# Kernel optimization log

Measured on AMD Instinct MI355X. Metric: run time of the kernel, lower is better.

The kernel has to match this reference:

```python
import jax, jax.numpy as jnp
import numpy as np

N_NODES = 100000
N_EDGES = 1600000
N_GRAPHS = 512
N_REL = 4
N_TYPES = 13
EMB = 128
HID = 128
BN_EPS = 1e-5
L2_EPS = 1e-12


def setup_inputs() -> dict:
    key = jax.random.key(0)
    ks = jax.random.split(key, 16)
    node_type = jax.random.randint(ks[0], (N_NODES,), 0, N_TYPES)
    x = jax.nn.one_hot(node_type, N_TYPES, dtype=jnp.float32)  # [N,13] one-hot
    edge_index = jax.random.randint(ks[1], (2, N_EDGES), 0, N_NODES)
    edge_type = jax.random.randint(ks[2], (N_EDGES,), 0, N_REL)
    batch = jnp.sort(jax.random.randint(ks[3], (N_NODES,), 0, N_GRAPHS))
    s = 0.05
    return {
        "x": x,
        "edge_index": edge_index,
        "edge_type": edge_type,
        "batch": batch,
        "emb": jax.random.normal(ks[4], (N_TYPES, EMB), jnp.float32) * s,
        "Wrel": jax.random.normal(ks[5], (2, N_REL, HID, HID), jnp.float32) * s,  # layer0 in=EMB==HID
        "Wroot": jax.random.normal(ks[6], (2, HID, HID), jnp.float32) * s,
        "conv_bias": jnp.zeros((2, HID), jnp.float32),
        "bn_gamma": jnp.ones((2, HID), jnp.float32),
        "bn_beta": jnp.zeros((2, HID), jnp.float32),
        "prelu_a": jnp.full((2,), 0.25, jnp.float32),
        "fc1_w": jax.random.normal(ks[7], (HID, 256), jnp.float32) * s,
        "fc1_b": jnp.zeros((256,), jnp.float32),
        "fc2_w": jax.random.normal(ks[8], (256, 128), jnp.float32) * s,
        "fc2_b": jnp.zeros((128,), jnp.float32),
        "out_w": jax.random.normal(ks[9], (128, 1), jnp.float32) * s,
        "out_b": jnp.zeros((1,), jnp.float32),
    }


def _rgcn_conv(h, Wrel, Wroot, bias, src, dst, edge_type):
    # PyG RGCNConv: out = h @ Wroot + bias + sum_r mean_{edges of rel r}(h_src @ W_r)
    n = h.shape[0]
    out = h @ Wroot + bias
    for r in range(N_REL):
        m = (edge_type == r).astype(h.dtype)  # [E]
        hr = h @ Wrel[r]                       # [N, dout]
        msg = hr[src] * m[:, None]             # gather + mask  [E, dout]
        num = jax.ops.segment_sum(msg, dst, num_segments=n)
        cnt = jax.ops.segment_sum(m, dst, num_segments=n)
        out = out + num / jnp.maximum(cnt, 1.0)[:, None]
    return out


def _batchnorm(h, gamma, beta):
    mu = jnp.mean(h, axis=0)
    var = jnp.mean((h - mu) ** 2, axis=0)  # biased var (training-mode BN)
    return (h - mu) * jax.lax.rsqrt(var + BN_EPS) * gamma + beta


def reference(x, edge_index, edge_type, batch, emb, Wrel, Wroot, conv_bias,
              bn_gamma, bn_beta, prelu_a, fc1_w, fc1_b, fc2_w, fc2_b, out_w, out_b):
    src, dst = edge_index[0], edge_index[1]
    idx = jnp.argmax(x, axis=1)         # torch.nonzero(one_hot)[1]
    h = emb[idx]                        # [N, EMB]
    for l in range(2):
        h = _rgcn_conv(h, Wrel[l], Wroot[l], conv_bias[l], src, dst, edge_type)
        h = _batchnorm(h, bn_gamma[l], bn_beta[l])
        h = jnp.where(h >= 0, h, prelu_a[l] * h)  # PReLU
        nrm = jnp.sqrt(jnp.sum(h * h, axis=1, keepdims=True))
        h = h / jnp.maximum(nrm, L2_EPS)          # F.normalize(p=2, dim=1)
    # global mean pool over graphs
    pooled = jax.ops.segment_sum(h, batch, num_segments=N_GRAPHS)
    cnt = jax.ops.segment_sum(jnp.ones((h.shape[0],), h.dtype), batch, num_segments=N_GRAPHS)
    g = pooled / jnp.maximum(cnt, 1.0)[:, None]   # [G, HID]
    g = jax.nn.relu(g @ fc1_w + fc1_b)
    g = jax.nn.relu(g @ fc2_w + fc2_b)
    return g @ out_w + out_b                      # [G, 1]
```

## Files before the change

kernel.cpp:

```cpp
#include <hip/hip_runtime.h>
#include <hip/hip_bf16.h>

#define NN 100000
#define NE 1600000
#define NG 512
#define CH3 65536
#define CHW 16384
#define NCH 2
#define BPC 128
#define ES 12500


typedef __attribute__((ext_vector_type(8))) short short8;
typedef __attribute__((ext_vector_type(4))) float float4v;


__device__ inline int lower_bound_dev(const int* __restrict__ a, int n, int v) {
    int lo = 0, hi = n;
    while (lo < hi) { int mid = (lo + hi) >> 1; if (a[mid] < v) lo = mid + 1; else hi = mid; }
    return lo;
}

__device__ inline unsigned short f2bf(float x) {
    unsigned u = __float_as_uint(x);
    unsigned r = (u + 0x7fffu + ((u >> 16) & 1u)) >> 16;
    return (unsigned short)r;
}

__device__ inline float bf2f(unsigned short h) {
    return __uint_as_float((unsigned)h << 16);
}


__global__ void node_type_kernel(const float* __restrict__ x, int* __restrict__ idx, int n) {
    int i = blockIdx.x * blockDim.x + threadIdx.x;
    if (i >= n) return;
    const float* row = x + (size_t)i * 13;
    int b = 0;
    #pragma unroll
    for (int t = 0; t < 13; ++t) if (row[t] > 0.5f) { b = t; }
    idx[i] = b;
}

__global__ void pack_src_type(const int* __restrict__ src, const int* __restrict__ ntype,
                              int* __restrict__ srcT) {
    int e = blockIdx.x * 256 + threadIdx.x;
    if (e >= NE) return;
    int s = src[e];
    srcT[e] = s | (ntype[s] << 17);
}


__global__ __launch_bounds__(256) void hist_kernel(const int* __restrict__ dst,
                                                   unsigned* __restrict__ partials) {
    __shared__ unsigned h[CHW];
    const int b = blockIdx.x, c = blockIdx.y;
    const int lo = c * CH3;
    for (int i = threadIdx.x; i < CHW; i += 256) h[i] = 0;
    __syncthreads();
    const int e0 = b * ES;
    const int e1 = (e0 + ES < NE) ? e0 + ES : NE;
    for (int e = e0 + threadIdx.x; e < e1; e += 256) {
        int k = dst[e] - lo;
        if (k >= 0 && k < CH3) atomicAdd(&h[k >> 2], 1u << ((k & 3) << 3));
    }
    __syncthreads();
    unsigned* out = partials + ((size_t)(c * BPC + b)) * CHW;
    for (int i = threadIdx.x; i < CHW; i += 256) out[i] = h[i];
}

__global__ void hist_reduce(unsigned* __restrict__ partials, int* __restrict__ counts) {
    const int c = blockIdx.y;
    const int i = blockIdx.x * 256 + threadIdx.x;
    size_t base = (size_t)c * BPC * CHW + i;
    unsigned r0 = 0, r1 = 0, r2 = 0, r3 = 0;
    #pragma unroll 4
    for (int b = 0; b < BPC; ++b) {
        unsigned t = partials[base + (size_t)b * CHW];
        partials[base + (size_t)b * CHW] = r0 | (r1 << 8) | (r2 << 16) | (r3 << 24);
        r0 += t & 0xffu; r1 += (t >> 8) & 0xffu; r2 += (t >> 16) & 0xffu; r3 += t >> 24;
    }
    int k0 = c * CH3 + 4 * i;
    if (k0 < NN)     counts[k0]     = (int)r0;
    if (k0 + 1 < NN) counts[k0 + 1] = (int)r1;
    if (k0 + 2 < NN) counts[k0 + 2] = (int)r2;
    if (k0 + 3 < NN) counts[k0 + 3] = (int)r3;
}

__global__ __launch_bounds__(256) void scan1(const int* __restrict__ counts, int* __restrict__ offs,
                                             int* __restrict__ bsums, int n) {
    __shared__ int wsum[4];
    const int base = blockIdx.x * 1024 + threadIdx.x * 4;
    int v[4]; int loc = 0;
    #pragma unroll
    for (int j = 0; j < 4; ++j) { int idx = base + j; v[j] = (idx < n) ? counts[idx] : 0; loc += v[j]; }
    const int lane = threadIdx.x & 63, wid = threadIdx.x >> 6;
    int sc = loc;
    #pragma unroll
    for (int o = 1; o < 64; o <<= 1) { int t = __shfl_up(sc, o, 64); if (lane >= o) sc += t; }
    if (lane == 63) wsum[wid] = sc;
    __syncthreads();
    int wbase = 0;
    for (int w = 0; w < wid; ++w) wbase += wsum[w];
    int run = wbase + sc - loc;
    #pragma unroll
    for (int j = 0; j < 4; ++j) { int idx = base + j; if (idx < n) offs[idx] = run; run += v[j]; }
    if (threadIdx.x == 255) bsums[blockIdx.x] = wbase + sc;
}

__global__ void scan2(int* __restrict__ bsums, int* __restrict__ offs, int nb, int n) {
    const int lane = threadIdx.x;
    int carry = 0;
    for (int base = 0; base < nb; base += 64) {
        int idx = base + lane;
        int v = (idx < nb) ? bsums[idx] : 0;
        int sc = v;
        #pragma unroll
        for (int o = 1; o < 64; o <<= 1) { int t = __shfl_up(sc, o, 64); if (lane >= o) sc += t; }
        if (idx < nb) bsums[idx] = carry + sc - v;
        int tot = __shfl(sc, 63, 64);
        carry += tot;
    }
    if (lane == 0) offs[n] = carry;
}

__global__ __launch_bounds__(256) void scan3(int* __restrict__ offs, const int* __restrict__ bsums, int n) {
    const int s = bsums[blockIdx.x];
    const int base = blockIdx.x * 1024 + threadIdx.x * 4;
    #pragma unroll
    for (int j = 0; j < 4; ++j) { int idx = base + j; if (idx < n) offs[idx] += s; }
}

__global__ __launch_bounds__(256) void place_kernel(const int* __restrict__ dst,
                                                    const int* __restrict__ et,
                                                    const int* __restrict__ srcT,
                                                    const int* __restrict__ offs,
                                                    const unsigned* __restrict__ partials,
                                                    int* __restrict__ sortedSrc) {
    __shared__ unsigned cur[CHW];
    const int b = blockIdx.x, c = blockIdx.y;
    const int lo = c * CH3;
    const unsigned* pb = partials + ((size_t)(c * BPC + b)) * CHW;
    for (int i = threadIdx.x; i < CHW; i += 256) cur[i] = pb[i];
    __syncthreads();
    const int e0 = b * ES;
    const int e1 = (e0 + ES < NE) ? e0 + ES : NE;
    for (int e = e0 + threadIdx.x; e < e1; e += 256) {
        int key = dst[e];
        int k = key - lo;
        if (k >= 0 && k < CH3) {
            int sh = (k & 3) << 3;
            unsigned old = atomicAdd(&cur[k >> 2], 1u << sh);
            int my = (int)((old >> sh) & 0xffu);
            int pos = offs[key] + my;
            sortedSrc[pos] = srcT[e] | (et[e] << 21);
        }
    }
}


__global__ __launch_bounds__(256) void hist_A0(const int* __restrict__ sortedSrc,
                                               const int* __restrict__ offs,
                                               const int* __restrict__ ntype,
                                               unsigned short* __restrict__ A0) {
    __shared__ unsigned cnt[256][13];
    const int tid = threadIdx.x;
    const int n = blockIdx.x * 256 + tid;
    if (n >= NN) return;
    #pragma unroll
    for (int t = 0; t < 13; ++t) cnt[tid][t] = 0;
    const int o0 = offs[n], o1 = offs[n + 1];
    unsigned relc = 0;
    for (int i = o0; i < o1; ++i) {
        int v = sortedSrc[i];
        int ty = (v >> 17) & 15, r = v >> 21;
        cnt[tid][ty] += 1u << (r << 3);
        relc += 1u << (r << 3);
    }
    float inv[4];
    #pragma unroll
    for (int r = 0; r < 4; ++r) {
        unsigned c = (relc >> (r << 3)) & 0xffu;
        inv[r] = 1.0f / (float)(c > 0 ? c : 1);
    }
    const int myty = ntype[n];
    const int tile = n >> 4, l16 = n & 15;
    unsigned short* base = A0 + (size_t)tile * 1536 + l16 * 8;
    #pragma unroll
    for (int ks = 0; ks < 3; ++ks) {
        #pragma unroll
        for (int quad = 0; quad < 4; ++quad) {
            unsigned short vals[8];
            #pragma unroll
            for (int j = 0; j < 8; ++j) {
                int p = ks * 32 + quad * 8 + j;
                float v;
                if (p < 32) v = (p == myty) ? 1.0f : 0.0f;
                else {
                    int r = (p - 32) >> 4, tt = (p - 32) & 15;
                    v = (tt < 13) ? (float)((cnt[tid][tt] >> (r << 3)) & 0xffu) * inv[r] : 0.0f;
                }
                vals[j] = f2bf(v);
            }
            *(uint4*)(base + ks * 512 + quad * 128) = *(uint4*)vals;
        }
    }
}


__global__ void build_B0(const float* __restrict__ emb, const float* __restrict__ Wroot,
                         const float* __restrict__ Wrel, unsigned short* __restrict__ B0f,
                         float* __restrict__ bnSums) {
    if (blockIdx.x < 8) bnSums[blockIdx.x * 256 + threadIdx.x] = 0.f;
    int i = blockIdx.x * 256 + threadIdx.x;
    if (i >= 12288) return;
    int j = i & 7;
    int lane = (i >> 3) & 63;
    int t = (i >> 9) & 7;
    int ks = i >> 12;
    int n = t * 16 + (lane & 15);
    int p = ks * 32 + (lane >> 4) * 8 + j;
    float val = 0.f;
    if (p < 32) {
        if (p < 13) {
            const float* er = emb + (size_t)p * 128;
            const float* wc = Wroot + n;
            float acc = 0.f;
            for (int k = 0; k < 128; ++k) acc += er[k] * wc[(size_t)k * 128];
            val = acc;
        }
    } else {
        int r = (p - 32) >> 4, tt = (p - 32) & 15;
        if (tt < 13) {
            const float* er = emb + (size_t)tt * 128;
            const float* wc = Wrel + ((size_t)r * 128) * 128 + n;
            float acc = 0.f;
            for (int k = 0; k < 128; ++k) acc += er[k] * wc[(size_t)k * 128];
            val = acc;
        }
    }
    B0f[i] = f2bf(val);
}


__global__ void build_Bf1(const float* __restrict__ Wroot, const float* __restrict__ Wrel,
                          unsigned short* __restrict__ Bf, float* __restrict__ bnSums) {
    if (blockIdx.x < 8) bnSums[blockIdx.x * 256 + threadIdx.x] = 0.f;
    int i = blockIdx.x * 256 + threadIdx.x;
    if (i >= 81920) return;
    int j = i & 7;
    int lane = (i >> 3) & 63;
    int t = (i >> 9) & 7;
    int ks = (i >> 12) & 3;
    int kc = i >> 14;
    int n = t * 16 + (lane & 15);
    int kcol = j * 16 + ks * 4 + (lane >> 4);
    float w;
    if (kc == 0) w = Wroot[16384 + (size_t)kcol * 128 + n];
    else {
        int r = kc - 1;
        w = Wrel[(((size_t)(4 + r) * 128) + kcol) * 128 + n];
    }
    Bf[i] = f2bf(w);
}


__global__ __launch_bounds__(256) void gemm0_mfma(const unsigned short* __restrict__ A0,
                                                  const unsigned short* __restrict__ B0f,
                                                  const float* __restrict__ bias,
                                                  unsigned short* __restrict__ Cb,
                                                  float* __restrict__ bnSums, int M) {
    __shared__ float sred[2][4][128];
    const int tid = threadIdx.x;
    const int wv = tid >> 6, lane = tid & 63;
    const int l16 = lane & 15, quad = lane >> 4;
    const int rowbase = blockIdx.x * 128 + wv * 32;
    const int tmax = (M >> 4) - 1;
    int tile0 = blockIdx.x * 8 + wv * 2; if (tile0 > tmax) tile0 = tmax;
    int tile1 = tile0 + 1;               if (tile1 > tmax) tile1 = tmax;

    float4v acc[2][8];
    #pragma unroll
    for (int t = 0; t < 8; ++t) {
        float bv = bias[t * 16 + l16];
        float4v av = {bv, bv, bv, bv};
        acc[0][t] = av; acc[1][t] = av;
    }

    const unsigned short* bl = B0f + lane * 8;
    const unsigned short* F0 = A0 + (size_t)tile0 * 1536 + quad * 128 + l16 * 8;
    const unsigned short* F1 = A0 + (size_t)tile1 * 1536 + quad * 128 + l16 * 8;
    #pragma unroll
    for (int ks = 0; ks < 3; ++ks) {
        short8 af0 = *(const short8*)(F0 + ks * 512);
        short8 af1 = *(const short8*)(F1 + ks * 512);
        const unsigned short* bp = bl + ((ks * 8) << 9);
        #pragma unroll
        for (int t = 0; t < 8; ++t) {
            short8 bf = *(const short8*)(bp + (t << 9));
            acc[0][t] = __builtin_amdgcn_mfma_f32_16x16x32_bf16(af0, bf, acc[0][t], 0, 0, 0);
            acc[1][t] = __builtin_amdgcn_mfma_f32_16x16x32_bf16(af1, bf, acc[1][t], 0, 0, 0);
        }
    }

    #pragma unroll
    for (int h = 0; h < 2; ++h) {
        #pragma unroll
        for (int rg = 0; rg < 4; ++rg) {
            int rr = rowbase + h * 16 + quad * 4 + rg;
            if (rr < M) {
                unsigned short v[8];
                #pragma unroll
                for (int t = 0; t < 8; ++t) v[t] = f2bf(acc[h][t][rg]);
                *(uint4*)(Cb + (size_t)rr * 128 + l16 * 8) = *(uint4*)v;
            }
        }
    }
    float s[8], q[8];
    #pragma unroll
    for (int t = 0; t < 8; ++t) {
        s[t] = 0.f; q[t] = 0.f;
        #pragma unroll
        for (int h = 0; h < 2; ++h) {
            #pragma unroll
            for (int rg = 0; rg < 4; ++rg) {
                int rr = rowbase + h * 16 + quad * 4 + rg;
                if (rr < M) { float v = acc[h][t][rg]; s[t] += v; q[t] += v * v; }
            }
        }
    }
    #pragma unroll
    for (int t = 0; t < 8; ++t) {
        s[t] += __shfl_down(s[t], 32, 64); q[t] += __shfl_down(q[t], 32, 64);
        s[t] += __shfl_down(s[t], 16, 64); q[t] += __shfl_down(q[t], 16, 64);
    }
    if (lane < 16) {
        #pragma unroll
        for (int t = 0; t < 8; ++t) {
            sred[0][wv][t * 16 + l16] = s[t];
            sred[1][wv][t * 16 + l16] = q[t];
        }
    }
    __syncthreads();
    if (tid < 128) {
        float S = sred[0][0][tid] + sred[0][1][tid] + sred[0][2][tid] + sred[0][3][tid];
        float Q = sred[1][0][tid] + sred[1][1][tid] + sred[1][2][tid] + sred[1][3][tid];
        float* bnS = bnSums + ((blockIdx.x & 7) << 8);
        unsafeAtomicAdd(bnS + tid, S);
        unsafeAtomicAdd(bnS + 128 + tid, Q);
    }
}


__global__ __launch_bounds__(256) void gather_gemm1(const unsigned short* __restrict__ hbf,
                                                    const int* __restrict__ sortedSrc,
                                                    const int* __restrict__ offs,
                                                    const unsigned short* __restrict__ Bf,
                                                    const float* __restrict__ bias,
                                                    unsigned short* __restrict__ Cb,
                                                    float* __restrict__ bnSums) {
    __shared__ unsigned short rootL[2048];
    __shared__ unsigned short aggL[8192];
    const int tid = threadIdx.x;
    const int tile = blockIdx.x;
    {
        const int l16g = tid >> 4;
        const int cidx = tid & 15;
        const int c8 = cidx << 3;
        const int n = tile * 16 + l16g;
        const int pu = cidx * 16 + (l16g ^ cidx);
        uint4 ru = *(const uint4*)(hbf + (size_t)n * 128 + c8);
        *(uint4*)(rootL + pu * 8) = ru;

        const unsigned short* hb = hbf + c8;
        const int o0 = offs[n], o1 = offs[n + 1];

        float a0[8], a1[8], a2[8], a3[8];
        #pragma unroll
        for (int j = 0; j < 8; ++j) { a0[j] = 0.f; a1[j] = 0.f; a2[j] = 0.f; a3[j] = 0.f; }
        float c0 = 0.f, c1 = 0.f, c2 = 0.f, c3 = 0.f;

        auto body = [&](int v, uint4 u) {
            int r = v >> 21;
            float f[8];
            f[0] = __uint_as_float(u.x << 16); f[1] = __uint_as_float(u.x & 0xffff0000u);
            f[2] = __uint_as_float(u.y << 16); f[3] = __uint_as_float(u.y & 0xffff0000u);
            f[4] = __uint_as_float(u.z << 16); f[5] = __uint_as_float(u.z & 0xffff0000u);
            f[6] = __uint_as_float(u.w << 16); f[7] = __uint_as_float(u.w & 0xffff0000u);
            float m0 = (r == 0) ? 1.f : 0.f, m1 = (r == 1) ? 1.f : 0.f;
            float m2 = (r == 2) ? 1.f : 0.f, m3 = (r == 3) ? 1.f : 0.f;
            c0 += m0; c1 += m1; c2 += m2; c3 += m3;
            #pragma unroll
            for (int j = 0; j < 8; ++j) {
                a0[j] = fmaf(m0, f[j], a0[j]);
                a1[j] = fmaf(m1, f[j], a1[j]);
                a2[j] = fmaf(m2, f[j], a2[j]);
                a3[j] = fmaf(m3, f[j], a3[j]);
            }
        };

        int i = o0;
        for (; i + 4 <= o1; i += 4) {
            int v0 = sortedSrc[i], v1 = sortedSrc[i + 1];
            int v2 = sortedSrc[i + 2], v3 = sortedSrc[i + 3];
            uint4 u0 = *(const uint4*)(hb + (size_t)(v0 & 0x1ffff) * 128);
            uint4 u1 = *(const uint4*)(hb + (size_t)(v1 & 0x1ffff) * 128);
            uint4 u2 = *(const uint4*)(hb + (size_t)(v2 & 0x1ffff) * 128);
            uint4 u3 = *(const uint4*)(hb + (size_t)(v3 & 0x1ffff) * 128);
            body(v0, u0); body(v1, u1); body(v2, u2); body(v3, u3);
        }
        if (i + 2 <= o1) {
            int v0 = sortedSrc[i], v1 = sortedSrc[i + 1];
            uint4 u0 = *(const uint4*)(hb + (size_t)(v0 & 0x1ffff) * 128);
            uint4 u1 = *(const uint4*)(hb + (size_t)(v1 & 0x1ffff) * 128);
            body(v0, u0); body(v1, u1);
            i += 2;
        }
        if (i < o1) {
            int v0 = sortedSrc[i];
            uint4 u0 = *(const uint4*)(hb + (size_t)(v0 & 0x1ffff) * 128);
            body(v0, u0);
        }

        const float i0 = 1.f / fmaxf(c0, 1.f), i1 = 1.f / fmaxf(c1, 1.f);
        const float i2 = 1.f / fmaxf(c2, 1.f), i3 = 1.f / fmaxf(c3, 1.f);
        unsigned short* bp = aggL + pu * 8;
        auto pack = [&](float* a, float inv, unsigned short* dp) {
            unsigned short v[8];
            #pragma unroll
            for (int j = 0; j < 8; ++j) v[j] = f2bf(a[j] * inv);
            *(uint4*)dp = *(uint4*)v;
        };
        pack(a0, i0, bp);
        pack(a1, i1, bp + 2048);
        pack(a2, i2, bp + 4096);
        pack(a3, i3, bp + 6144);
    }
    __syncthreads();

    const int wv = tid >> 6, lane = tid & 63;
    const int l16 = lane & 15, quad = lane >> 4;
    const int t0 = wv << 1;
    float4v acc0, acc1;
    {
        float b0v = bias[t0 * 16 + l16];
        float b1v = bias[(t0 + 1) * 16 + l16];
        float4v a0v = {b0v, b0v, b0v, b0v};
        float4v a1v = {b1v, b1v, b1v, b1v};
        acc0 = a0v; acc1 = a1v;
    }
    const unsigned short* bl = Bf + lane * 8;
    #pragma unroll
    for (int kc = 0; kc < 5; ++kc) {
        const unsigned short* Abase = (kc == 0) ? rootL : (aggL + (kc - 1) * 2048);
        #pragma unroll
        for (int ks = 0; ks < 4; ++ks) {
            const int C = ks * 4 + quad;
            const int p = C * 16 + (l16 ^ C);
            short8 af = *(const short8*)(Abase + p * 8);
            const unsigned short* bp = bl + (((kc * 4 + ks) * 8 + t0) << 9);
            short8 b0 = *(const short8*)(bp);
            short8 b1 = *(const short8*)(bp + 512);
            acc0 = __builtin_amdgcn_mfma_f32_16x16x32_bf16(af, b0, acc0, 0, 0, 0);
            acc1 = __builtin_amdgcn_mfma_f32_16x16x32_bf16(af, b1, acc1, 0, 0, 0);
        }
    }
    const int rowbase = tile * 16;
    #pragma unroll
    for (int rg = 0; rg < 4; ++rg) {
        int rr = rowbase + quad * 4 + rg;
        unsigned pk = (unsigned)f2bf(acc0[rg]) | ((unsigned)f2bf(acc1[rg]) << 16);
        *(unsigned*)(Cb + (size_t)rr * 128 + l16 * 8 + t0) = pk;
    }
    float s0 = 0.f, q0 = 0.f, s1 = 0.f, q1 = 0.f;
    #pragma unroll
    for (int rg = 0; rg < 4; ++rg) {
        float v0 = acc0[rg], v1 = acc1[rg];
        s0 += v0; q0 += v0 * v0; s1 += v1; q1 += v1 * v1;
    }
    s0 += __shfl_down(s0, 32, 64); q0 += __shfl_down(q0, 32, 64);
    s1 += __shfl_down(s1, 32, 64); q1 += __shfl_down(q1, 32, 64);
    s0 += __shfl_down(s0, 16, 64); q0 += __shfl_down(q0, 16, 64);
    s1 += __shfl_down(s1, 16, 64); q1 += __shfl_down(q1, 16, 64);
    if (lane < 16) {
        float* bnS = bnSums + ((tile & 7) << 8);
        unsafeAtomicAdd(bnS + t0 * 16 + l16, s0);
        unsafeAtomicAdd(bnS + 128 + t0 * 16 + l16, q0);
        unsafeAtomicAdd(bnS + (t0 + 1) * 16 + l16, s1);
        unsafeAtomicAdd(bnS + 128 + (t0 + 1) * 16 + l16, q1);
    }
}


__global__ void bn_finalize(const float* __restrict__ bnSums, float* __restrict__ fin,
                            float* __restrict__ g0zero, int n) {
    const int c = threadIdx.x;
    if (g0zero) g0zero[blockIdx.x * 128 + c] = 0.f;
    if (blockIdx.x != 0) return;
    float s = 0.f, q = 0.f;
    #pragma unroll
    for (int j = 0; j < 8; ++j) { s += bnSums[j * 256 + c]; q += bnSums[j * 256 + 128 + c]; }
    const float invn = 1.0f / (float)n;
    float mu = s * invn;
    float var = q * invn - mu * mu; if (var < 0.f) var = 0.f;
    fin[c] = mu;
    fin[128 + c] = rsqrtf(var + 1e-5f);
}


__global__ __launch_bounds__(256) void bn_apply_kernel(const unsigned short* __restrict__ Cb,
                                unsigned short* __restrict__ hbf,
                                const float* __restrict__ fin,
                                const float* __restrict__ gamma, const float* __restrict__ beta,
                                const float* __restrict__ prelu_a, int layer) {
    const int tid = threadIdx.x;
    const int row = blockIdx.x * 16 + (tid >> 4);
    const int li = tid & 15;
    const int p8 = li << 3;
    const float a = prelu_a[layer];
    uint4 u = *(const uint4*)(Cb + (size_t)row * 128 + p8);
    float v[8];
    v[0] = __uint_as_float(u.x << 16); v[1] = __uint_as_float(u.x & 0xffff0000u);
    v[2] = __uint_as_float(u.y << 16); v[3] = __uint_as_float(u.y & 0xffff0000u);
    v[4] = __uint_as_float(u.z << 16); v[5] = __uint_as_float(u.z & 0xffff0000u);
    v[6] = __uint_as_float(u.w << 16); v[7] = __uint_as_float(u.w & 0xffff0000u);
    float t[8]; float ss = 0.f;
    #pragma unroll
    for (int j = 0; j < 8; ++j) {
        int cc = j * 16 + li;
        float tv = (v[j] - fin[cc]) * fin[128 + cc] * gamma[cc] + beta[cc];
        tv = (tv >= 0.f) ? tv : a * tv;
        t[j] = tv; ss += tv * tv;
    }
    ss += __shfl_xor(ss, 1, 64);
    ss += __shfl_xor(ss, 2, 64);
    ss += __shfl_xor(ss, 4, 64);
    ss += __shfl_xor(ss, 8, 64);
    const float scale = 1.0f / fmaxf(sqrtf(ss), 1e-12f);
    unsigned short o[8];
    #pragma unroll
    for (int j = 0; j < 8; ++j) o[j] = f2bf(t[j] * scale);
    *(uint4*)(hbf + (size_t)row * 128 + p8) = *(uint4*)o;
}


__global__ __launch_bounds__(256) void bn_apply_pool(const unsigned short* __restrict__ Cb,
                                const float* __restrict__ fin,
                                const float* __restrict__ gamma, const float* __restrict__ beta,
                                const float* __restrict__ prelu_a,
                                const int* __restrict__ batch,
                                float* __restrict__ g0) {
    __shared__ float P[16][128];
    __shared__ int gids[16];
    const int tid = threadIdx.x;
    const int r16 = tid >> 4;
    const int li = tid & 15;
    const int row = blockIdx.x * 16 + r16;
    const int p8 = li << 3;
    if (li == 0) gids[r16] = batch[row];
    const float a = prelu_a[1];
    uint4 u = *(const uint4*)(Cb + (size_t)row * 128 + p8);
    float v[8];
    v[0] = __uint_as_float(u.x << 16); v[1] = __uint_as_float(u.x & 0xffff0000u);
    v[2] = __uint_as_float(u.y << 16); v[3] = __uint_as_float(u.y & 0xffff0000u);
    v[4] = __uint_as_float(u.z << 16); v[5] = __uint_as_float(u.z & 0xffff0000u);
    v[6] = __uint_as_float(u.w << 16); v[7] = __uint_as_float(u.w & 0xffff0000u);
    float t[8]; float ss = 0.f;
    #pragma unroll
    for (int j = 0; j < 8; ++j) {
        int cc = j * 16 + li;
        float tv = (v[j] - fin[cc]) * fin[128 + cc] * gamma[cc] + beta[cc];
        tv = (tv >= 0.f) ? tv : a * tv;
        t[j] = tv; ss += tv * tv;
    }
    ss += __shfl_xor(ss, 1, 64);
    ss += __shfl_xor(ss, 2, 64);
    ss += __shfl_xor(ss, 4, 64);
    ss += __shfl_xor(ss, 8, 64);
    const float scale = 1.0f / fmaxf(sqrtf(ss), 1e-12f);
    #pragma unroll
    for (int j = 0; j < 8; ++j) P[r16][p8 + j] = t[j] * scale;
    __syncthreads();
    if (tid < 128) {
        int cur = gids[0];
        float run = 0.f;
        #pragma unroll
        for (int rr = 0; rr < 16; ++rr) {
            int g = gids[rr];
            if (g != cur) {
                unsafeAtomicAdd(&g0[(size_t)cur * 128 + tid], run);
                run = 0.f; cur = g;
            }
            run += P[rr][tid];
        }
        unsafeAtomicAdd(&g0[(size_t)cur * 128 + tid], run);
    }
}


__global__ void fc1_kernel(const float* __restrict__ g, const float* __restrict__ w,
                           const float* __restrict__ b, const int* __restrict__ batch,
                           float* __restrict__ o) {
    const int row = blockIdx.x;
    const int j = threadIdx.x;
    const int lo = lower_bound_dev(batch, NN, row);
    const int hi = lower_bound_dev(batch, NN, row + 1);
    const int c = hi - lo;
    const float invc = 1.0f / (float)(c > 0 ? c : 1);
    float acc = 0.f;
    #pragma unroll 8
    for (int k = 0; k < 128; ++k) {
        int lk = (k & 7) * 16 + (k >> 3);
        acc += g[row * 128 + k] * w[lk * 256 + j];
    }
    o[row * 256 + j] = fmaxf(acc * invc + b[j], 0.f);
}

__global__ void fc2_kernel(const float* __restrict__ g, const float* __restrict__ w,
                           const float* __restrict__ b, float* __restrict__ o) {
    const int row = blockIdx.x;
    const int j = threadIdx.x;
    float acc = b[j];
    #pragma unroll 8
    for (int k = 0; k < 256; ++k) acc += g[row * 256 + k] * w[k * 128 + j];
    o[row * 128 + j] = fmaxf(acc, 0.f);
}

__global__ void fco_kernel(const float* __restrict__ g, const float* __restrict__ w,
                           const float* __restrict__ b, float* __restrict__ o) {
    const int row = blockIdx.x * blockDim.x + threadIdx.x;
    if (row >= NG) return;
    float acc = b[0];
    #pragma unroll 8
    for (int k = 0; k < 128; ++k) acc += g[row * 128 + k] * w[k];
    o[row] = acc;
}


extern "C" void kernel_launch(void* const* d_in, const int* in_sizes, int n_in,
                              void* d_out, int out_size, void* d_ws, size_t ws_size,
                              hipStream_t stream) {
    const float* x      = (const float*)d_in[0];
    const int*   eidx   = (const int*)d_in[1];
    const int*   etype  = (const int*)d_in[2];
    const int*   batch  = (const int*)d_in[3];
    const float* emb    = (const float*)d_in[4];
    const float* Wrel   = (const float*)d_in[5];
    const float* Wroot  = (const float*)d_in[6];
    const float* cbias  = (const float*)d_in[7];
    const float* gamma  = (const float*)d_in[8];
    const float* beta   = (const float*)d_in[9];
    const float* prelua = (const float*)d_in[10];
    const float* fc1w   = (const float*)d_in[11];
    const float* fc1b   = (const float*)d_in[12];
    const float* fc2w   = (const float*)d_in[13];
    const float* fc2b   = (const float*)d_in[14];
    const float* outw   = (const float*)d_in[15];
    const float* outb   = (const float*)d_in[16];
    float* out = (float*)d_out;

    const int* src = eidx;
    const int* dst = eidx + NE;

    char* p = (char*)d_ws;
    auto alloc = [&](size_t bytes) { char* r = p; p += (bytes + 255) & ~(size_t)255; return r; };
    unsigned short* hbf   = (unsigned short*)alloc((size_t)NN * 128 * 2);
    unsigned short* Cb    = (unsigned short*)alloc((size_t)NN * 128 * 2);
    char*  scratch   = (char*)alloc((size_t)24 << 20);
    int*   sortedSrc = (int*)alloc((size_t)NE * 4);
    int*   srcT      = (int*)alloc((size_t)NE * 4);
    int*   offs      = (int*)alloc((size_t)(NN + 1) * 4);
    int*   bsums     = (int*)alloc(1024);
    int*   ntype     = (int*)alloc((size_t)NN * 4);
    unsigned short* Bf1 = (unsigned short*)alloc((size_t)81920 * 2);
    unsigned short* B0f = (unsigned short*)alloc((size_t)12288 * 2);
    float* bnSums  = (float*)alloc(2048 * 4);
    float* bnFin   = (float*)alloc(256 * 4);
    float* g0      = (float*)alloc((size_t)NG * 128 * 4);
    float* g1      = (float*)alloc((size_t)NG * 256 * 4);
    float* g2      = (float*)alloc((size_t)NG * 128 * 4);

    unsigned* partials = (unsigned*)scratch;
    unsigned short* A0 = (unsigned short*)scratch;

    const int NBLK = (NN + 1023) / 1024;

    node_type_kernel<<<(NN + 255) / 256, 256, 0, stream>>>(x, ntype, NN);
    pack_src_type<<<(NE + 255) / 256, 256, 0, stream>>>(src, ntype, srcT);

    hist_kernel<<<dim3(BPC, NCH), 256, 0, stream>>>(dst, partials);
    hist_reduce<<<dim3(CHW / 256, NCH), 256, 0, stream>>>(partials, offs);
    scan1<<<NBLK, 256, 0, stream>>>(offs, offs, bsums, NN);
    scan2<<<1, 64, 0, stream>>>(bsums, offs, NBLK, NN);
    scan3<<<NBLK, 256, 0, stream>>>(offs, bsums, NN);
    place_kernel<<<dim3(BPC, NCH), 256, 0, stream>>>(dst, etype, srcT, offs, partials, sortedSrc);

    hist_A0<<<(NN + 255) / 256, 256, 0, stream>>>(sortedSrc, offs, ntype, A0);

    build_B0<<<48, 256, 0, stream>>>(emb, Wroot, Wrel, B0f, bnSums);
    gemm0_mfma<<<(NN + 127) / 128, 256, 0, stream>>>(A0, B0f, cbias, Cb, bnSums, NN);
    bn_finalize<<<1, 128, 0, stream>>>(bnSums, bnFin, (float*)nullptr, NN);
    bn_apply_kernel<<<NN / 16, 256, 0, stream>>>(Cb, hbf, bnFin, gamma, beta, prelua, 0);

    build_Bf1<<<320, 256, 0, stream>>>(Wroot, Wrel, Bf1, bnSums);
    gather_gemm1<<<NN / 16, 256, 0, stream>>>(hbf, sortedSrc, offs, Bf1, cbias + 128, Cb, bnSums);
    bn_finalize<<<512, 128, 0, stream>>>(bnSums, bnFin, g0, NN);
    bn_apply_pool<<<NN / 16, 256, 0, stream>>>(Cb, bnFin, gamma + 128, beta + 128,
                                               prelua, batch, g0);

    fc1_kernel<<<NG, 256, 0, stream>>>(g0, fc1w, fc1b, batch, g1);
    fc2_kernel<<<NG, 128, 0, stream>>>(g1, fc2w, fc2b, g2);
    fco_kernel<<<2, 256, 0, stream>>>(g2, outw, outb, out);
}
```

Baseline: 374.8 us.

## Fuse per-node type histogram into layer-0 GEMM and merge setup kernels

Moves the per-node neighbour type/relation histogram (hist_A0) into the layer-0 MFMA GEMM, so the A0 operand is built in shared memory instead of written to and re-read from global memory. Folds pack_src_type into the chunk-0 blocks of hist_kernel, including the edge type in the packed word, and drops the et read from place_kernel. Merges the two weight-packing kernels into one launch and adds a bn_finalize0 that zeroes bnSums after use. This removes several launches and a global round trip. In exchange, only half the GEMM block's threads build the A tile, serially over each node's edges, before the MFMA loop starts.

```diff
diff --git a/kernel.cpp b/kernel.cpp
--- a/kernel.cpp
+++ b/kernel.cpp
@@ -42,16 +42,65 @@
     idx[i] = b;
 }
 
-__global__ void pack_src_type(const int* __restrict__ src, const int* __restrict__ ntype,
-                              int* __restrict__ srcT) {
-    int e = blockIdx.x * 256 + threadIdx.x;
-    if (e >= NE) return;
-    int s = src[e];
-    srcT[e] = s | (ntype[s] << 17);
+
+__global__ void build_weights(const float* __restrict__ emb, const float* __restrict__ Wroot,
+                              const float* __restrict__ Wrel,
+                              unsigned short* __restrict__ Bf, unsigned short* __restrict__ B0f,
+                              float* __restrict__ bnSums) {
+    if (blockIdx.x < 8) bnSums[blockIdx.x * 256 + threadIdx.x] = 0.f;
+    int i = blockIdx.x * 256 + threadIdx.x;
+    if (i < 81920) {
+        int j = i & 7;
+        int lane = (i >> 3) & 63;
+        int t = (i >> 9) & 7;
+        int ks = (i >> 12) & 3;
+        int kc = i >> 14;
+        int n = t * 16 + (lane & 15);
+        int kcol = j * 16 + ks * 4 + (lane >> 4);
+        float w;
+        if (kc == 0) w = Wroot[16384 + (size_t)kcol * 128 + n];
+        else {
+            int r = kc - 1;
+            w = Wrel[(((size_t)(4 + r) * 128) + kcol) * 128 + n];
+        }
+        Bf[i] = f2bf(w);
+    } else {
+        int i0 = i - 81920;
+        int j = i0 & 7;
+        int lane = (i0 >> 3) & 63;
+        int t = (i0 >> 9) & 7;
+        int ks = i0 >> 12;
+        int n = t * 16 + (lane & 15);
+        int p = ks * 32 + (lane >> 4) * 8 + j;
+        float val = 0.f;
+        if (p < 32) {
+            if (p < 13) {
+                const float* er = emb + (size_t)p * 128;
+                const float* wc = Wroot + n;
+                float acc = 0.f;
+                for (int k = 0; k < 128; ++k) acc += er[k] * wc[(size_t)k * 128];
+                val = acc;
+            }
+        } else {
+            int r = (p - 32) >> 4, tt = (p - 32) & 15;
+            if (tt < 13) {
+                const float* er = emb + (size_t)tt * 128;
+                const float* wc = Wrel + ((size_t)r * 128) * 128 + n;
+                float acc = 0.f;
+                for (int k = 0; k < 128; ++k) acc += er[k] * wc[(size_t)k * 128];
+                val = acc;
+            }
+        }
+        B0f[i0] = f2bf(val);
+    }
 }
 
 
 __global__ __launch_bounds__(256) void hist_kernel(const int* __restrict__ dst,
+                                                   const int* __restrict__ src,
+                                                   const int* __restrict__ et,
+                                                   const int* __restrict__ ntype,
+                                                   int* __restrict__ srcT,
                                                    unsigned* __restrict__ partials) {
     __shared__ unsigned h[CHW];
     const int b = blockIdx.x, c = blockIdx.y;
@@ -60,9 +109,18 @@
     __syncthreads();
     const int e0 = b * ES;
     const int e1 = (e0 + ES < NE) ? e0 + ES : NE;
-    for (int e = e0 + threadIdx.x; e < e1; e += 256) {
-        int k = dst[e] - lo;
-        if (k >= 0 && k < CH3) atomicAdd(&h[k >> 2], 1u << ((k & 3) << 3));
+    if (c == 0) {
+        for (int e = e0 + threadIdx.x; e < e1; e += 256) {
+            int k = dst[e] - lo;
+            if (k >= 0 && k < CH3) atomicAdd(&h[k >> 2], 1u << ((k & 3) << 3));
+            int s = src[e];
+            srcT[e] = s | (ntype[s] << 17) | (et[e] << 21);
+        }
+    } else {
+        for (int e = e0 + threadIdx.x; e < e1; e += 256) {
+            int k = dst[e] - lo;
+            if (k >= 0 && k < CH3) atomicAdd(&h[k >> 2], 1u << ((k & 3) << 3));
+        }
     }
     __syncthreads();
     unsigned* out = partials + ((size_t)(c * BPC + b)) * CHW;
@@ -132,7 +190,6 @@
 }
 
 __global__ __launch_bounds__(256) void place_kernel(const int* __restrict__ dst,
-                                                    const int* __restrict__ et,
                                                     const int* __restrict__ srcT,
                                                     const int* __restrict__ offs,
                                                     const unsigned* __restrict__ partials,
@@ -153,131 +210,78 @@
             unsigned old = atomicAdd(&cur[k >> 2], 1u << sh);
             int my = (int)((old >> sh) & 0xffu);
             int pos = offs[key] + my;
-            sortedSrc[pos] = srcT[e] | (et[e] << 21);
-        }
-    }
-}
-
-
-__global__ __launch_bounds__(256) void hist_A0(const int* __restrict__ sortedSrc,
-                                               const int* __restrict__ offs,
-                                               const int* __restrict__ ntype,
-                                               unsigned short* __restrict__ A0) {
-    __shared__ unsigned cnt[256][13];
-    const int tid = threadIdx.x;
-    const int n = blockIdx.x * 256 + tid;
-    if (n >= NN) return;
-    #pragma unroll
-    for (int t = 0; t < 13; ++t) cnt[tid][t] = 0;
-    const int o0 = offs[n], o1 = offs[n + 1];
-    unsigned relc = 0;
-    for (int i = o0; i < o1; ++i) {
-        int v = sortedSrc[i];
-        int ty = (v >> 17) & 15, r = v >> 21;
-        cnt[tid][ty] += 1u << (r << 3);
-        relc += 1u << (r << 3);
-    }
-    float inv[4];
-    #pragma unroll
-    for (int r = 0; r < 4; ++r) {
-        unsigned c = (relc >> (r << 3)) & 0xffu;
-        inv[r] = 1.0f / (float)(c > 0 ? c : 1);
-    }
-    const int myty = ntype[n];
-    const int tile = n >> 4, l16 = n & 15;
-    unsigned short* base = A0 + (size_t)tile * 1536 + l16 * 8;
-    #pragma unroll
-    for (int ks = 0; ks < 3; ++ks) {
-        #pragma unroll
-        for (int quad = 0; quad < 4; ++quad) {
-            unsigned short vals[8];
-            #pragma unroll
-            for (int j = 0; j < 8; ++j) {
-                int p = ks * 32 + quad * 8 + j;
-                float v;
-                if (p < 32) v = (p == myty) ? 1.0f : 0.0f;
-                else {
-                    int r = (p - 32) >> 4, tt = (p - 32) & 15;
-                    v = (tt < 13) ? (float)((cnt[tid][tt] >> (r << 3)) & 0xffu) * inv[r] : 0.0f;
-                }
-                vals[j] = f2bf(v);
-            }
-            *(uint4*)(base + ks * 512 + quad * 128) = *(uint4*)vals;
-        }
-    }
-}
-
-
-__global__ void build_B0(const float* __restrict__ emb, const float* __restrict__ Wroot,
-                         const float* __restrict__ Wrel, unsigned short* __restrict__ B0f,
-                         float* __restrict__ bnSums) {
-    if (blockIdx.x < 8) bnSums[blockIdx.x * 256 + threadIdx.x] = 0.f;
-    int i = blockIdx.x * 256 + threadIdx.x;
-    if (i >= 12288) return;
-    int j = i & 7;
-    int lane = (i >> 3) & 63;
-    int t = (i >> 9) & 7;
-    int ks = i >> 12;
-    int n = t * 16 + (lane & 15);
-    int p = ks * 32 + (lane >> 4) * 8 + j;
-    float val = 0.f;
-    if (p < 32) {
-        if (p < 13) {
-            const float* er = emb + (size_t)p * 128;
-            const float* wc = Wroot + n;
-            float acc = 0.f;
-            for (int k = 0; k < 128; ++k) acc += er[k] * wc[(size_t)k * 128];
-            val = acc;
-        }
-    } else {
-        int r = (p - 32) >> 4, tt = (p - 32) & 15;
-        if (tt < 13) {
-            const float* er = emb + (size_t)tt * 128;
-            const float* wc = Wrel + ((size_t)r * 128) * 128 + n;
-            float acc = 0.f;
-            for (int k = 0; k < 128; ++k) acc += er[k] * wc[(size_t)k * 128];
-            val = acc;
-        }
-    }
-    B0f[i] = f2bf(val);
-}
-
-
-__global__ void build_Bf1(const float* __restrict__ Wroot, const float* __restrict__ Wrel,
-                          unsigned short* __restrict__ Bf, float* __restrict__ bnSums) {
-    if (blockIdx.x < 8) bnSums[blockIdx.x * 256 + threadIdx.x] = 0.f;
-    int i = blockIdx.x * 256 + threadIdx.x;
-    if (i >= 81920) return;
-    int j = i & 7;
-    int lane = (i >> 3) & 63;
-    int t = (i >> 9) & 7;
-    int ks = (i >> 12) & 3;
-    int kc = i >> 14;
-    int n = t * 16 + (lane & 15);
-    int kcol = j * 16 + ks * 4 + (lane >> 4);
-    float w;
-    if (kc == 0) w = Wroot[16384 + (size_t)kcol * 128 + n];
-    else {
-        int r = kc - 1;
-        w = Wrel[(((size_t)(4 + r) * 128) + kcol) * 128 + n];
-    }
-    Bf[i] = f2bf(w);
-}
-
-
-__global__ __launch_bounds__(256) void gemm0_mfma(const unsigned short* __restrict__ A0,
-                                                  const unsigned short* __restrict__ B0f,
-                                                  const float* __restrict__ bias,
-                                                  unsigned short* __restrict__ Cb,
-                                                  float* __restrict__ bnSums, int M) {
+            sortedSrc[pos] = srcT[e];
+        }
+    }
+}
+
+
+__global__ __launch_bounds__(256) void gemm0_fused(const int* __restrict__ sortedSrc,
+                                                   const int* __restrict__ offs,
+                                                   const int* __restrict__ ntype,
+                                                   const unsigned short* __restrict__ B0f,
+                                                   const float* __restrict__ bias,
+                                                   unsigned short* __restrict__ Cb,
+                                                   float* __restrict__ bnSums, int M) {
+    __shared__ unsigned short A0L[12 * 128 * 8];
+    __shared__ unsigned cnt[128][13];
     __shared__ float sred[2][4][128];
     const int tid = threadIdx.x;
+
+    if (tid < 128) {
+        const int n = blockIdx.x * 128 + tid;
+        const int tile = tid >> 4, l16 = tid & 15;
+        if (n < M) {
+            #pragma unroll
+            for (int t = 0; t < 13; ++t) cnt[tid][t] = 0;
+            const int o0 = offs[n], o1 = offs[n + 1];
+            unsigned relc = 0;
+            for (int i = o0; i < o1; ++i) {
+                int v = sortedSrc[i];
+                int ty = (v >> 17) & 15, r = v >> 21;
+                cnt[tid][ty] += 1u << (r << 3);
+                relc += 1u << (r << 3);
+            }
+            float inv[4];
+            #pragma unroll
+            for (int r = 0; r < 4; ++r) {
+                unsigned c = (relc >> (r << 3)) & 0xffu;
+                inv[r] = 1.0f / (float)(c > 0 ? c : 1);
+            }
+            const int myty = ntype[n];
+            #pragma unroll
+            for (int ks = 0; ks < 3; ++ks) {
+                #pragma unroll
+                for (int quad = 0; quad < 4; ++quad) {
+                    unsigned short vals[8];
+                    #pragma unroll
+                    for (int j = 0; j < 8; ++j) {
+                        int p = ks * 32 + quad * 8 + j;
+                        float v;
+                        if (p < 32) v = (p == myty) ? 1.0f : 0.0f;
+                        else {
+                            int r = (p - 32) >> 4, tt = (p - 32) & 15;
+                            v = (tt < 13) ? (float)((cnt[tid][tt] >> (r << 3)) & 0xffu) * inv[r] : 0.0f;
+                        }
+                        vals[j] = f2bf(v);
+                    }
+                    const int C = ks * 4 + quad;
+                    *(uint4*)(A0L + (C * 128 + tile * 16 + l16) * 8) = *(uint4*)vals;
+                }
+            }
+        } else {
+            uint4 z; z.x = 0; z.y = 0; z.z = 0; z.w = 0;
+            #pragma unroll
+            for (int C = 0; C < 12; ++C)
+                *(uint4*)(A0L + (C * 128 + tile * 16 + l16) * 8) = z;
+        }
+    }
+    __syncthreads();
+
     const int wv = tid >> 6, lane = tid & 63;
     const int l16 = lane & 15, quad = lane >> 4;
     const int rowbase = blockIdx.x * 128 + wv * 32;
-    const int tmax = (M >> 4) - 1;
-    int tile0 = blockIdx.x * 8 + wv * 2; if (tile0 > tmax) tile0 = tmax;
-    int tile1 = tile0 + 1;               if (tile1 > tmax) tile1 = tmax;
+    const int tileL0 = wv * 2, tileL1 = wv * 2 + 1;
 
     float4v acc[2][8];
     #pragma unroll
@@ -288,12 +292,11 @@
     }
 
     const unsigned short* bl = B0f + lane * 8;
-    const unsigned short* F0 = A0 + (size_t)tile0 * 1536 + quad * 128 + l16 * 8;
-    const unsigned short* F1 = A0 + (size_t)tile1 * 1536 + quad * 128 + l16 * 8;
     #pragma unroll
     for (int ks = 0; ks < 3; ++ks) {
-        short8 af0 = *(const short8*)(F0 + ks * 512);
-        short8 af1 = *(const short8*)(F1 + ks * 512);
+        const int C = ks * 4 + quad;
+        short8 af0 = *(const short8*)(A0L + (C * 128 + tileL0 * 16 + l16) * 8);
+        short8 af1 = *(const short8*)(A0L + (C * 128 + tileL1 * 16 + l16) * 8);
         const unsigned short* bp = bl + ((ks * 8) << 9);
         #pragma unroll
         for (int t = 0; t < 8; ++t) {
@@ -489,6 +492,23 @@
         unsafeAtomicAdd(bnS + (t0 + 1) * 16 + l16, s1);
         unsafeAtomicAdd(bnS + 128 + (t0 + 1) * 16 + l16, q1);
     }
+}
+
+
+__global__ void bn_finalize0(float* __restrict__ bnSums, float* __restrict__ fin, int n) {
+    const int c = threadIdx.x;
+    if (c < 128) {
+        float s = 0.f, q = 0.f;
+        #pragma unroll
+        for (int j = 0; j < 8; ++j) { s += bnSums[j * 256 + c]; q += bnSums[j * 256 + 128 + c]; }
+        const float invn = 1.0f / (float)n;
+        float mu = s * invn;
+        float var = q * invn - mu * mu; if (var < 0.f) var = 0.f;
+        fin[c] = mu;
+        fin[128 + c] = rsqrtf(var + 1e-5f);
+    }
+    __syncthreads();
+    for (int i = c; i < 2048; i += 256) bnSums[i] = 0.f;
 }
 
 
@@ -666,7 +686,7 @@
     auto alloc = [&](size_t bytes) { char* r = p; p += (bytes + 255) & ~(size_t)255; return r; };
     unsigned short* hbf   = (unsigned short*)alloc((size_t)NN * 128 * 2);
     unsigned short* Cb    = (unsigned short*)alloc((size_t)NN * 128 * 2);
-    char*  scratch   = (char*)alloc((size_t)24 << 20);
+    unsigned* partials = (unsigned*)alloc((size_t)NCH * BPC * CHW * 4);
     int*   sortedSrc = (int*)alloc((size_t)NE * 4);
     int*   srcT      = (int*)alloc((size_t)NE * 4);
     int*   offs      = (int*)alloc((size_t)(NN + 1) * 4);
@@ -680,29 +700,23 @@
     float* g1      = (float*)alloc((size_t)NG * 256 * 4);
     float* g2      = (float*)alloc((size_t)NG * 128 * 4);
 
-    unsigned* partials = (unsigned*)scratch;
-    unsigned short* A0 = (unsigned short*)scratch;
-
     const int NBLK = (NN + 1023) / 1024;
 
     node_type_kernel<<<(NN + 255) / 256, 256, 0, stream>>>(x, ntype, NN);
-    pack_src_type<<<(NE + 255) / 256, 256, 0, stream>>>(src, ntype, srcT);
-
-    hist_kernel<<<dim3(BPC, NCH), 256, 0, stream>>>(dst, partials);
+    build_weights<<<368, 256, 0, stream>>>(emb, Wroot, Wrel, Bf1, B0f, bnSums);
+
+    hist_kernel<<<dim3(BPC, NCH), 256, 0, stream>>>(dst, src, etype, ntype, srcT, partials);
     hist_reduce<<<dim3(CHW / 256, NCH), 256, 0, stream>>>(partials, offs);
     scan1<<<NBLK, 256, 0, stream>>>(offs, offs, bsums, NN);
     scan2<<<1, 64, 0, stream>>>(bsums, offs, NBLK, NN);
     scan3<<<NBLK, 256, 0, stream>>>(offs, bsums, NN);
-    place_kernel<<<dim3(BPC, NCH), 256, 0, stream>>>(dst, etype, srcT, offs, partials, sortedSrc);
-
-    hist_A0<<<(NN + 255) / 256, 256, 0, stream>>>(sortedSrc, offs, ntype, A0);
-
-    build_B0<<<48, 256, 0, stream>>>(emb, Wroot, Wrel, B0f, bnSums);
-    gemm0_mfma<<<(NN + 127) / 128, 256, 0, stream>>>(A0, B0f, cbias, Cb, bnSums, NN);
-    bn_finalize<<<1, 128, 0, stream>>>(bnSums, bnFin, (float*)nullptr, NN);
+    place_kernel<<<dim3(BPC, NCH), 256, 0, stream>>>(dst, srcT, offs, partials, sortedSrc);
+
+    gemm0_fused<<<(NN + 127) / 128, 256, 0, stream>>>(sortedSrc, offs, ntype, B0f,
+                                                      cbias, Cb, bnSums, NN);
+    bn_finalize0<<<1, 256, 0, stream>>>(bnSums, bnFin, NN);
     bn_apply_kernel<<<NN / 16, 256, 0, stream>>>(Cb, hbf, bnFin, gamma, beta, prelua, 0);
 
-    build_Bf1<<<320, 256, 0, stream>>>(Wroot, Wrel, Bf1, bnSums);
     gather_gemm1<<<NN / 16, 256, 0, stream>>>(hbf, sortedSrc, offs, Bf1, cbias + 128, Cb, bnSums);
     bn_finalize<<<512, 128, 0, stream>>>(bnSums, bnFin, g0, NN);
     bn_apply_pool<<<NN / 16, 256, 0, stream>>>(Cb, bnFin, gamma + 128, beta + 128,
```

Result: faster. 359.0 us (-4.2%).
